# Kernel optimization log

Hardware: AMD Instinct MI355X
Metric: run time of the kernel (lower is better)

The kernel has to match this reference:

```python
import jax, jax.numpy as jnp
import numpy as np

A = 32        # num_agents (nodes per graph block)
B = 128       # batch graphs
N = B * A     # nodes per timestep = 4096
T = 5         # temporal_window_size
K = 16        # num_belief_states
AD = 8        # action_dim
H = 4         # num_attn_heads
DH = 64       # hidden_dim (per GAT head)
D = H * DH    # feature_dim = 256
HD = D // H   # temporal MHA head dim = 64
L = 64        # latent_dim
FIN = K + AD  # discrete node feature dim = 24


def _block_edges():
    # fully connected within each batch block, incl. self loops (PyG GATConv default)
    s = np.repeat(np.arange(A), A)
    d = np.tile(np.arange(A), A)
    off = (np.arange(B) * A)[:, None]
    src = (off + s[None, :]).reshape(-1)
    dst = (off + d[None, :]).reshape(-1)
    return jnp.asarray(np.stack([src, dst]), dtype=jnp.int32)  # [2, B*A*A]


def setup_inputs():
    key = jax.random.key(0)
    ks = jax.random.split(key, 16)
    g = lambda i, shape, s=0.05: jax.random.normal(ks[i], shape, dtype=jnp.float32) * s
    z = lambda shape: jnp.zeros(shape, jnp.float32)
    return {
        'node_feats': g(0, (T, N, FIN), 1.0),
        'edge_index': _block_edges(),
        'gat1_w': g(1, (FIN, D)), 'gat1_asrc': g(2, (H, DH)), 'gat1_adst': g(3, (H, DH)), 'gat1_b': z((D,)),
        'gat2_w': g(4, (D, D)), 'gat2_asrc': g(5, (H, DH)), 'gat2_adst': g(6, (H, DH)), 'gat2_b': z((D,)),
        'wq': g(7, (D, D)), 'bq': z((D,)),
        'wk': g(8, (D, D)), 'bk': z((D,)),
        'wv': g(9, (D, D)), 'bv': z((D,)),
        'wo': g(10, (D, D)), 'bo': z((D,)),
        'lm_w': g(11, (D, L)), 'lm_b': z((L,)),
        'lv_w': g(12, (D, L)), 'lv_b': z((L,)),
        'ap_w': g(13, (L, AD * A)), 'ap_b': z((AD * A,)),
        'bh_w': g(14, (D, K)), 'bh_b': z((K,)),
    }


def _gat_layer(x, W, a_src, a_dst, b, src, dst):
    # PyG GATConv: per-edge additive attention, softmax over incoming edges of dst
    h = (x @ W).reshape(N, H, DH)
    al_s = (h * a_src[None]).sum(-1)                      # [N,H]
    al_d = (h * a_dst[None]).sum(-1)                      # [N,H]
    e = jax.nn.leaky_relu(al_s[src] + al_d[dst], 0.2)     # [E,H]
    m = jax.ops.segment_max(e, dst, num_segments=N)
    p = jnp.exp(e - m[dst])
    zden = jax.ops.segment_sum(p, dst, num_segments=N)
    alpha = p / (zden[dst] + 1e-16)                       # [E,H]
    out = jax.ops.segment_sum(h[src] * alpha[:, :, None], dst, num_segments=N)
    return out.reshape(N, D) + b


def reference(node_feats, edge_index, gat1_w, gat1_asrc, gat1_adst, gat1_b,
              gat2_w, gat2_asrc, gat2_adst, gat2_b,
              wq, bq, wk, bk, wv, bv, wo, bo,
              lm_w, lm_b, lv_w, lv_b, ap_w, ap_b, bh_w, bh_b):
    src, dst = edge_index[0], edge_index[1]

    def gnn(x):  # two GATConv layers + ReLU (dropout inactive at inference)
        x = jax.nn.relu(_gat_layer(x, gat1_w, gat1_asrc, gat1_adst, gat1_b, src, dst))
        x = jax.nn.relu(_gat_layer(x, gat2_w, gat2_asrc, gat2_adst, gat2_b, src, dst))
        return x

    feats = jax.vmap(gnn)(node_feats)          # [T,N,D]
    ego = feats[:, ::A, :]                     # ego node of each block -> [T,B,D]
    seq = jnp.transpose(ego, (1, 0, 2))        # [B,T,D]

    # temporal MultiheadAttention with causal mask (batch_first)
    q = (seq @ wq + bq).reshape(B, T, H, HD)
    k = (seq @ wk + bk).reshape(B, T, H, HD)
    v = (seq @ wv + bv).reshape(B, T, H, HD)
    scores = jnp.einsum('bthd,bshd->bhts', q, k) / jnp.sqrt(jnp.float32(HD))
    causal = jnp.tril(jnp.ones((T, T), bool))
    scores = jnp.where(causal[None, None], scores, jnp.float32(-1e9))
    attn = jax.nn.softmax(scores, axis=-1)
    ctx = jnp.einsum('bhts,bshd->bthd', attn, v).reshape(B, T, D)
    feat = (ctx @ wo + bo)[:, -1]              # last timestep features [B,D]

    mu = feat @ lm_w + lm_b                    # latent_mean
    logvar = feat @ lv_w + lv_b                # latent_logvar
    act = mu @ ap_w + ap_b                     # action_predictor(latent)
    belief = feat @ bh_w + bh_b                # belief_head(features)
    return jnp.concatenate([mu, logvar, act, belief], axis=-1)  # [B, 2L+AD*A+K]
```

## Files before the change

kernel.cpp:

```cpp
#include <hip/hip_runtime.h>

typedef unsigned short u16;
typedef unsigned int u32;
typedef short bf16x8 __attribute__((ext_vector_type(8)));
typedef float f32x4  __attribute__((ext_vector_type(4)));


__device__ __forceinline__ u16 f2b(float f) {
    unsigned u = __float_as_uint(f);
    return (u16)((u + 0x7FFFu + ((u >> 16) & 1u)) >> 16);
}
__device__ __forceinline__ float b2f(u16 u) {
    return __uint_as_float(((unsigned)u) << 16);
}
__device__ __forceinline__ u32 pk2(float a, float b) {
    return (u32)f2b(a) | ((u32)f2b(b) << 16);
}

__global__ __launch_bounds__(256) void prep_kernel(
    const float* __restrict__ w2, u16* __restrict__ w2t,
    const float* __restrict__ w1, u16* __restrict__ w1t)
{
    if (blockIdx.x == 64) {
        const int n = threadIdx.x;
        u32 pk[16];
#pragma unroll
        for (int s = 0; s < 16; ++s) {
            const int k = 2 * s;
            const float lo = (k < 24)     ? w1[k * 256 + n]       : 0.f;
            const float hi = (k + 1 < 24) ? w1[(k + 1) * 256 + n] : 0.f;
            pk[s] = pk2(lo, hi);
        }
        u32* dst = (u32*)(w1t + n * 32);
#pragma unroll
        for (int s = 0; s < 4; ++s)
            *(uint4*)&dst[s * 4] = make_uint4(pk[4*s], pk[4*s+1], pk[4*s+2], pk[4*s+3]);
        return;
    }
    __shared__ float tile[32][33];
    const int bi = blockIdx.x >> 3, bj = blockIdx.x & 7;
    const int r0 = bi * 32, c0 = bj * 32;
    const int lr = threadIdx.x >> 5, lc = threadIdx.x & 31;
    for (int i = lr; i < 32; i += 8)
        tile[i][lc] = w2[(r0 + i) * 256 + c0 + lc];
    __syncthreads();
    for (int i = lr; i < 32; i += 8)
        w2t[(c0 + i) * 256 + r0 + lc] = f2b(tile[lc][i]);
}

__global__ __launch_bounds__(256, 3) void gat12_kernel(
    const float* __restrict__ x, const u16* __restrict__ w1t,
    const float* __restrict__ a1s, const float* __restrict__ a1d,
    const float* __restrict__ b1,
    const u16* __restrict__ w2t, const float* __restrict__ a2s,
    const float* __restrict__ a2d, const float* __restrict__ b2,
    u16* __restrict__ ego,
    const float* __restrict__ wq, const float* __restrict__ wk,
    const float* __restrict__ wv, const float* __restrict__ wo,
    const float* __restrict__ lm_w, const float* __restrict__ lv_w,
    const float* __restrict__ bh_w, const float* __restrict__ ap_w,
    u16* __restrict__ wqkvt, u16* __restrict__ wot,
    u16* __restrict__ headT, u16* __restrict__ apT)
{
    constexpr int HP = 40;
    constexpr int XP = 264;

    __shared__ u16 h1T[256 * HP];
    __shared__ u16 x2s[32 * XP];
    __shared__ u16 alphaT[4 * 32 * HP];
    __shared__ float als2[256], ald2[256];
    __shared__ u16 a1sb[256], a1db[256], a2sb[256], a2db[256];
    __shared__ float alpha0[4][32];

    const int tid = threadIdx.x;

    if (blockIdx.x >= 640) {
        const int bid = blockIdx.x - 640;
        const float* src; u16* dst;
        int C = 256, S = 256, roff = 0, bi, bj;
        if (bid < 192) {
            const int m = bid >> 6, tl = bid & 63;
            src = (m == 0) ? wq : (m == 1) ? wk : wv;
            dst = wqkvt + m * 65536;
            bi = tl >> 3; bj = tl & 7;
        } else if (bid < 256) {
            const int tl = bid - 192;
            src = wo; dst = wot; bi = tl >> 3; bj = tl & 7;
        } else if (bid < 272) {
            const int tl = bid - 256;
            src = lm_w; dst = headT; C = 64; bi = tl >> 1; bj = tl & 1;
        } else if (bid < 288) {
            const int tl = bid - 272;
            src = lv_w; dst = headT; C = 64; roff = 64; bi = tl >> 1; bj = tl & 1;
        } else if (bid < 296) {
            src = bh_w; dst = headT; C = 16; roff = 128; bi = bid - 288; bj = 0;
        } else {
            const int tl = bid - 296;
            src = ap_w; dst = apT; S = 64; bi = tl >> 3; bj = tl & 7;
        }
        float (*tile)[33] = (float(*)[33])h1T;
        const int r0 = bi * 32, c0 = bj * 32;
        const int lr = tid >> 5, lc = tid & 31;
        const int cw = (C - c0 < 32) ? (C - c0) : 32;
        for (int i = lr; i < 32; i += 8)
            if (lc < cw) tile[i][lc] = src[(r0 + i) * C + c0 + lc];
        __syncthreads();
        for (int i = lr; i < cw; i += 8)
            dst[(roff + c0 + i) * S + r0 + lc] = f2b(tile[lc][i]);
        return;
    }

    const int wave = tid >> 6;
    const int l    = tid & 63;
    const int l15  = l & 15;
    const int quad = l >> 4;
    const int t    = blockIdx.x >> 7;
    const int b    = blockIdx.x & 127;
    const long row0 = (long)(t * 4096 + b * 32);

    u16* xs = alphaT;
    if (tid < 128) {
        const int node = tid >> 2, seg = tid & 3;
        u32 pk[4] = {0, 0, 0, 0};
        if (seg < 3) {
            const float* xp = x + row0 * 24 + node * 24 + seg * 8;
            const float4 v0 = *(const float4*)xp;
            const float4 v1 = *(const float4*)(xp + 4);
            pk[0] = pk2(v0.x, v0.y); pk[1] = pk2(v0.z, v0.w);
            pk[2] = pk2(v1.x, v1.y); pk[3] = pk2(v1.z, v1.w);
        }
        *(uint4*)&xs[node * 32 + seg * 8] = make_uint4(pk[0], pk[1], pk[2], pk[3]);
    }
    a1sb[tid] = f2b(a1s[tid]);  a1db[tid] = f2b(a1d[tid]);
    a2sb[tid] = f2b(a2s[tid]);  a2db[tid] = f2b(a2d[tid]);
    __syncthreads();

    {
        const int n0 = wave * 64;
        const bf16x8 a0 = *(const bf16x8*)&xs[(l15)      * 32 + quad * 8];
        const bf16x8 a1 = *(const bf16x8*)&xs[(16 + l15) * 32 + quad * 8];
        f32x4 acc[2][4];
#pragma unroll
        for (int nt = 0; nt < 4; ++nt) {
            const bf16x8 bb = *(const bf16x8*)(w1t + (n0 + nt * 16 + l15) * 32 + quad * 8);
            acc[0][nt] = __builtin_amdgcn_mfma_f32_16x16x32_bf16(a0, bb, (f32x4){0.f,0.f,0.f,0.f}, 0, 0, 0);
            acc[1][nt] = __builtin_amdgcn_mfma_f32_16x16x32_bf16(a1, bb, (f32x4){0.f,0.f,0.f,0.f}, 0, 0, 0);
        }
        __syncthreads();
#pragma unroll
        for (int mt = 0; mt < 2; ++mt)
#pragma unroll
            for (int nt = 0; nt < 4; ++nt) {
                const int col = n0 + nt * 16 + l15;
                *(uint2*)&h1T[col * HP + mt * 16 + quad * 4] =
                    make_uint2(pk2(acc[mt][nt][0], acc[mt][nt][1]),
                               pk2(acc[mt][nt][2], acc[mt][nt][3]));
            }
    }
    __syncthreads();

    {
        const int pair = tid >> 7;
        const int id = tid & 127;
        const int i = id >> 2, hh = id & 3;
        float as = 0.f, ad = 0.f;
        for (int cc = 0; cc < 32; ++cc) {
            const int c = (((cc + tid) & 31) | (pair << 5)) + hh * 64;
            const float hv = b2f(h1T[c * HP + i]);
            as += hv * b2f(a1sb[c]);
            ad += hv * b2f(a1db[c]);
        }
        als2[tid] = as;
        ald2[tid] = ad;
    }
    __syncthreads();

    if (tid < 128) {
        const int hh = tid & 3, dd = tid >> 2;
        const float advv = ald2[tid] + ald2[128 + tid];
        float e[32]; float m = -1e30f;
#pragma unroll
        for (int s = 0; s < 32; ++s) {
            float v = (als2[s * 4 + hh] + als2[128 + s * 4 + hh]) + advv;
            v = v > 0.f ? v : 0.2f * v;
            e[s] = v; m = fmaxf(m, v);
        }
        float sum = 0.f;
#pragma unroll
        for (int s = 0; s < 32; ++s) { float p = __expf(e[s] - m); e[s] = p; sum += p; }
        const float inv = 1.f / (sum + 1e-16f);
        u32 pk[16];
#pragma unroll
        for (int s = 0; s < 16; ++s) pk[s] = pk2(e[2*s] * inv, e[2*s+1] * inv);
        u32* dst = (u32*)&alphaT[(hh * 32 + dd) * HP];
#pragma unroll
        for (int s = 0; s < 4; ++s)
            *(uint4*)&dst[s * 4] = make_uint4(pk[4*s], pk[4*s+1], pk[4*s+2], pk[4*s+3]);
    }
    __syncthreads();

    {
        const int hh = wave;
        bf16x8 af[2];
#pragma unroll
        for (int mt = 0; mt < 2; ++mt)
            af[mt] = *(const bf16x8*)&alphaT[(hh * 32 + mt * 16 + l15) * HP + quad * 8];
        f32x4 acc[2][4];
#pragma unroll
        for (int mt = 0; mt < 2; ++mt)
#pragma unroll
            for (int nt = 0; nt < 4; ++nt) acc[mt][nt] = (f32x4){0.f, 0.f, 0.f, 0.f};
#pragma unroll
        for (int nt = 0; nt < 4; ++nt) {
            const bf16x8 bf = *(const bf16x8*)&h1T[(hh * 64 + nt * 16 + l15) * HP + quad * 8];
            acc[0][nt] = __builtin_amdgcn_mfma_f32_16x16x32_bf16(af[0], bf, acc[0][nt], 0, 0, 0);
            acc[1][nt] = __builtin_amdgcn_mfma_f32_16x16x32_bf16(af[1], bf, acc[1][nt], 0, 0, 0);
        }
#pragma unroll
        for (int mt = 0; mt < 2; ++mt)
#pragma unroll
            for (int nt = 0; nt < 4; ++nt) {
                const int col = hh * 64 + nt * 16 + l15;
                const float bb = b1[col];
#pragma unroll
                for (int r = 0; r < 4; ++r) {
                    const int d = mt * 16 + quad * 4 + r;
                    x2s[d * XP + col] = f2b(fmaxf(acc[mt][nt][r] + bb, 0.f));
                }
            }
    }
    __syncthreads();

    u16* h2s = h1T;
    {
        const int n0 = wave * 64;
        f32x4 acc[2][4];
#pragma unroll
        for (int mt = 0; mt < 2; ++mt)
#pragma unroll
            for (int nt = 0; nt < 4; ++nt) acc[mt][nt] = (f32x4){0.f, 0.f, 0.f, 0.f};
        for (int k0 = 0; k0 < 256; k0 += 32) {
            const int kb = k0 + quad * 8;
            const bf16x8 a0 = *(const bf16x8*)&x2s[(l15)      * XP + kb];
            const bf16x8 a1 = *(const bf16x8*)&x2s[(16 + l15) * XP + kb];
#pragma unroll
            for (int nt = 0; nt < 4; ++nt) {
                const bf16x8 bb = *(const bf16x8*)(w2t + (n0 + nt * 16 + l15) * 256 + kb);
                acc[0][nt] = __builtin_amdgcn_mfma_f32_16x16x32_bf16(a0, bb, acc[0][nt], 0, 0, 0);
                acc[1][nt] = __builtin_amdgcn_mfma_f32_16x16x32_bf16(a1, bb, acc[1][nt], 0, 0, 0);
            }
        }
#pragma unroll
        for (int mt = 0; mt < 2; ++mt)
#pragma unroll
            for (int nt = 0; nt < 4; ++nt) {
                const int col = n0 + nt * 16 + l15;
                *(uint2*)&h2s[col * HP + mt * 16 + quad * 4] =
                    make_uint2(pk2(acc[mt][nt][0], acc[mt][nt][1]),
                               pk2(acc[mt][nt][2], acc[mt][nt][3]));
            }
    }
    __syncthreads();

    {
        const int pair = tid >> 7;
        const int id = tid & 127;
        const int i = id >> 2, hh = id & 3;
        float as = 0.f, ad = 0.f;
        for (int cc = 0; cc < 32; ++cc) {
            const int c = (((cc + tid) & 31) | (pair << 5)) + hh * 64;
            const float hv = b2f(h2s[c * HP + i]);
            as += hv * b2f(a2sb[c]);
            if (i == 0) ad += hv * b2f(a2db[c]);
        }
        als2[tid] = as;
        if (i == 0) ald2[tid] = ad;
    }
    __syncthreads();

    if (tid < 4) {
        const int hh = tid;
        const float advv = ald2[hh] + ald2[128 + hh];
        float e[32]; float m = -1e30f;
#pragma unroll
        for (int s = 0; s < 32; ++s) {
            float v = (als2[s * 4 + hh] + als2[128 + s * 4 + hh]) + advv;
            v = v > 0.f ? v : 0.2f * v;
            e[s] = v; m = fmaxf(m, v);
        }
        float sum = 0.f;
#pragma unroll
        for (int s = 0; s < 32; ++s) { float p = __expf(e[s] - m); e[s] = p; sum += p; }
        const float inv = 1.f / (sum + 1e-16f);
#pragma unroll
        for (int s = 0; s < 32; ++s) alpha0[hh][s] = e[s] * inv;
    }
    __syncthreads();

    {
        const int hh = tid >> 6;
        float av[32];
#pragma unroll
        for (int j = 0; j < 8; ++j)
            *(float4*)&av[j * 4] = *(const float4*)&alpha0[hh][j * 4];
        const u32* hp = (const u32*)&h2s[tid * HP];
        float a = 0.f;
#pragma unroll
        for (int s2 = 0; s2 < 16; ++s2) {
            const u32 u = hp[s2];
            a += av[2 * s2]     * __uint_as_float(u << 16);
            a += av[2 * s2 + 1] * __uint_as_float(u & 0xffff0000u);
        }
        ego[((long)(t * 128 + b)) * 256 + tid] = f2b(fmaxf(a + b2[tid], 0.f));
    }
}

__global__ __launch_bounds__(256) void qkv_kernel(
    const u16* __restrict__ ego, const u16* __restrict__ wqkvt,
    const float* __restrict__ bq, const float* __restrict__ bk,
    const float* __restrict__ bv_, float* __restrict__ qkv)
{
    const int tid  = threadIdx.x;
    const int wave = tid >> 6;
    const int l    = tid & 63;
    const int l15  = l & 15;
    const int quad = l >> 4;
    int gx, gy;
    if (blockIdx.x < 20)      { gy = 1; gx = blockIdx.x; }
    else if (blockIdx.x < 40) { gy = 2; gx = blockIdx.x - 20; }
    else                      { gy = 0; gx = 16 + (blockIdx.x - 40); }
    const int r0 = gx * 32;
    const int n0 = wave * 64;
    const u16* wsrc = wqkvt + gy * 65536;
    const float* bias = (gy == 0) ? bq : (gy == 1) ? bk : bv_;

    f32x4 acc[2][4];
#pragma unroll
    for (int mt = 0; mt < 2; ++mt)
#pragma unroll
        for (int nt = 0; nt < 4; ++nt) acc[mt][nt] = (f32x4){0.f, 0.f, 0.f, 0.f};

    for (int k0 = 0; k0 < 256; k0 += 32) {
        const int kb = k0 + quad * 8;
        const bf16x8 a0 = *(const bf16x8*)(ego + (r0 + l15)      * 256 + kb);
        const bf16x8 a1 = *(const bf16x8*)(ego + (r0 + 16 + l15) * 256 + kb);
#pragma unroll
        for (int nt = 0; nt < 4; ++nt) {
            const bf16x8 bb = *(const bf16x8*)(wsrc + (n0 + nt * 16 + l15) * 256 + kb);
            acc[0][nt] = __builtin_amdgcn_mfma_f32_16x16x32_bf16(a0, bb, acc[0][nt], 0, 0, 0);
            acc[1][nt] = __builtin_amdgcn_mfma_f32_16x16x32_bf16(a1, bb, acc[1][nt], 0, 0, 0);
        }
    }
#pragma unroll
    for (int mt = 0; mt < 2; ++mt)
#pragma unroll
        for (int nt = 0; nt < 4; ++nt)
#pragma unroll
            for (int r = 0; r < 4; ++r) {
                const int row = r0 + mt * 16 + quad * 4 + r;
                const int col = n0 + nt * 16 + l15;
                qkv[(long)row * 768 + gy * 256 + col] = acc[mt][nt][r] + bias[col];
            }
}

__global__ __launch_bounds__(256) void attn_tail_kernel(
    const float* __restrict__ qkv,
    const u16* __restrict__ wot, const u16* __restrict__ headT,
    const u16* __restrict__ apT,
    const float* __restrict__ bo,
    const float* __restrict__ lm_b, const float* __restrict__ lv_b,
    const float* __restrict__ bh_b, const float* __restrict__ ap_b,
    float* __restrict__ out)
{
    constexpr int FP = 264;
    constexpr int MP = 72;
    __shared__ float scl[16][20];
    __shared__ u16 fs[16 * FP];
    __shared__ u16 ffs[16 * FP];
    __shared__ u16 mus[16 * MP];

    const int tid  = threadIdx.x;
    const int wave = tid >> 6;
    const int l    = tid & 63;
    const int l15  = l & 15;
    const int quad = l >> 4;
    const int b0   = blockIdx.x * 16;

    for (int id = tid; id < 320; id += 256) {
        const int bl = id / 20, r = id % 20, h = r / 5, s = r % 5;
        const float* qp = qkv + (long)(512 + b0 + bl) * 768 + h * 64;
        const float* kp = qkv + (long)(s * 128 + b0 + bl) * 768 + 256 + h * 64;
        float acc = 0.f;
        for (int c = 0; c < 64; c += 4) {
            const float4 qv = *(const float4*)(qp + c);
            const float4 kv = *(const float4*)(kp + c);
            acc += qv.x * kv.x + qv.y * kv.y + qv.z * kv.z + qv.w * kv.w;
        }
        scl[bl][r] = acc * 0.125f;
    }
    __syncthreads();

    if (tid < 64) {
        const int bl = tid >> 2, h = tid & 3;
        float m = -1e30f;
        for (int s = 0; s < 5; ++s) m = fmaxf(m, scl[bl][h * 5 + s]);
        float p[5], sum = 0.f;
        for (int s = 0; s < 5; ++s) { p[s] = __expf(scl[bl][h * 5 + s] - m); sum += p[s]; }
        for (int s = 0; s < 5; ++s) scl[bl][h * 5 + s] = p[s] / sum;
    }
    __syncthreads();

    {
        const int col = tid, h = col >> 6;
        for (int bl = 0; bl < 16; ++bl) {
            float c = 0.f;
#pragma unroll
            for (int s = 0; s < 5; ++s)
                c += scl[bl][h * 5 + s] * qkv[(long)(s * 128 + b0 + bl) * 768 + 512 + col];
            fs[bl * FP + col] = f2b(c);
        }
    }
    __syncthreads();

    {
        const int n0 = wave * 64;
        f32x4 acc[4];
#pragma unroll
        for (int nt = 0; nt < 4; ++nt) acc[nt] = (f32x4){0.f, 0.f, 0.f, 0.f};
        for (int k0 = 0; k0 < 256; k0 += 32) {
            const int kb = k0 + quad * 8;
            const bf16x8 a = *(const bf16x8*)&fs[l15 * FP + kb];
#pragma unroll
            for (int nt = 0; nt < 4; ++nt) {
                const bf16x8 bb = *(const bf16x8*)(wot + (n0 + nt * 16 + l15) * 256 + kb);
                acc[nt] = __builtin_amdgcn_mfma_f32_16x16x32_bf16(a, bb, acc[nt], 0, 0, 0);
            }
        }
#pragma unroll
        for (int nt = 0; nt < 4; ++nt) {
            const int col = n0 + nt * 16 + l15;
            const float bb = bo[col];
#pragma unroll
            for (int r = 0; r < 4; ++r)
                ffs[(quad * 4 + r) * FP + col] = f2b(acc[nt][r] + bb);
        }
    }
    __syncthreads();

    for (int nt = wave; nt < 9; nt += 4) {
        const int n0 = nt * 16;
        f32x4 acc = (f32x4){0.f, 0.f, 0.f, 0.f};
        for (int k0 = 0; k0 < 256; k0 += 32) {
            const int kb = k0 + quad * 8;
            const bf16x8 a  = *(const bf16x8*)&ffs[l15 * FP + kb];
            const bf16x8 bb = *(const bf16x8*)(headT + (n0 + l15) * 256 + kb);
            acc = __builtin_amdgcn_mfma_f32_16x16x32_bf16(a, bb, acc, 0, 0, 0);
        }
        const int col = n0 + l15;
#pragma unroll
        for (int r = 0; r < 4; ++r) {
            const int row = quad * 4 + r;
            float v = acc[r];
            if (col < 64) {
                v += lm_b[col];
                out[(long)(b0 + row) * 400 + col] = v;
                mus[row * MP + col] = f2b(v);
            } else if (col < 128) {
                v += lv_b[col - 64];
                out[(long)(b0 + row) * 400 + col] = v;
            } else {
                v += bh_b[col - 128];
                out[(long)(b0 + row) * 400 + 256 + col] = v;
            }
        }
    }
    __syncthreads();

#pragma unroll
    for (int i = 0; i < 4; ++i) {
        const int n0 = (wave * 4 + i) * 16;
        f32x4 acc = (f32x4){0.f, 0.f, 0.f, 0.f};
#pragma unroll
        for (int k0 = 0; k0 < 64; k0 += 32) {
            const int kb = k0 + quad * 8;
            const bf16x8 a  = *(const bf16x8*)&mus[l15 * MP + kb];
            const bf16x8 bb = *(const bf16x8*)(apT + (n0 + l15) * 64 + kb);
            acc = __builtin_amdgcn_mfma_f32_16x16x32_bf16(a, bb, acc, 0, 0, 0);
        }
        const int col = n0 + l15;
        const float bb = ap_b[col];
#pragma unroll
        for (int r = 0; r < 4; ++r) {
            const int row = quad * 4 + r;
            out[(long)(b0 + row) * 400 + 128 + col] = acc[r] + bb;
        }
    }
}

extern "C" void kernel_launch(void* const* d_in, const int* in_sizes, int n_in,
                              void* d_out, int out_size, void* d_ws, size_t ws_size,
                              hipStream_t stream)
{
    const float* node_feats = (const float*)d_in[0];
    const float* g1w  = (const float*)d_in[2];
    const float* g1as = (const float*)d_in[3];
    const float* g1ad = (const float*)d_in[4];
    const float* g1b  = (const float*)d_in[5];
    const float* g2w  = (const float*)d_in[6];
    const float* g2as = (const float*)d_in[7];
    const float* g2ad = (const float*)d_in[8];
    const float* g2b  = (const float*)d_in[9];
    const float* wq = (const float*)d_in[10]; const float* bq = (const float*)d_in[11];
    const float* wk = (const float*)d_in[12]; const float* bk = (const float*)d_in[13];
    const float* wv = (const float*)d_in[14]; const float* bv = (const float*)d_in[15];
    const float* wo = (const float*)d_in[16]; const float* bo = (const float*)d_in[17];
    const float* lm_w = (const float*)d_in[18]; const float* lm_b = (const float*)d_in[19];
    const float* lv_w = (const float*)d_in[20]; const float* lv_b = (const float*)d_in[21];
    const float* ap_w = (const float*)d_in[22]; const float* ap_b = (const float*)d_in[23];
    const float* bh_w = (const float*)d_in[24]; const float* bh_b = (const float*)d_in[25];

    char* ws = (char*)d_ws;
    u16*   ego   = (u16*)ws;
    u16*   w2t   = (u16*)(ws + 327680);
    u16*   w1t   = (u16*)(ws + 458752);
    u16*   wqkvt = (u16*)(ws + 475136);
    float* qkv   = (float*)(ws + 868352);
    u16*   wot   = (u16*)(ws + 2834432);
    u16*   headT = (u16*)(ws + 2965504);
    u16*   apT   = (u16*)(ws + 3039232);

    prep_kernel<<<65, 256, 0, stream>>>(g2w, w2t, g1w, w1t);
    gat12_kernel<<<952, 256, 0, stream>>>(node_feats, w1t, g1as, g1ad, g1b,
                                          w2t, g2as, g2ad, g2b, ego,
                                          wq, wk, wv, wo, lm_w, lv_w, bh_w, ap_w,
                                          wqkvt, wot, headT, apT);
    qkv_kernel<<<44, 256, 0, stream>>>(ego, wqkvt, bq, bk, bv, qkv);
    attn_tail_kernel<<<8, 256, 0, stream>>>(qkv, wot, headT, apT, bo,
                                            lm_b, lv_b, bh_b, ap_b, (float*)d_out);
}
```

Measured before the change: 156.9 us.

## Fuse QKV projection and attention tail into one per-graph kernel, shrink GAT LDS

Measured after the change: 162.2 us. 1.03x slower.

```diff
diff --git a/kernel.cpp b/kernel.cpp
--- a/kernel.cpp
+++ b/kernel.cpp
@@ -48,7 +48,7 @@
         w2t[(c0 + i) * 256 + r0 + lc] = f2b(tile[lc][i]);
 }
 
-__global__ __launch_bounds__(256, 3) void gat12_kernel(
+__global__ __launch_bounds__(256, 4) void gat12_kernel(
     const float* __restrict__ x, const u16* __restrict__ w1t,
     const float* __restrict__ a1s, const float* __restrict__ a1d,
     const float* __restrict__ b1,
@@ -65,13 +65,10 @@
     constexpr int HP = 40;
     constexpr int XP = 264;
 
-    __shared__ u16 h1T[256 * HP];
-    __shared__ u16 x2s[32 * XP];
-    __shared__ u16 alphaT[4 * 32 * HP];
-    __shared__ float als2[256], ald2[256];
-    __shared__ u16 a1sb[256], a1db[256], a2sb[256], a2db[256];
-    __shared__ float alpha0[4][32];
-
+    __shared__ __align__(16) u16 h1T[256 * HP];
+    __shared__ __align__(16) u16 x2s[32 * XP];
+    __shared__ float als[128], ald[128];
+    __shared__ __align__(16) u16 avec[1024];
     const int tid = threadIdx.x;
 
     if (blockIdx.x >= 640) {
@@ -110,6 +107,10 @@
         return;
     }
 
+    u16* xs     = x2s;
+    u16* alphaT = x2s;
+    float* alpha0 = (float*)avec;
+
     const int wave = tid >> 6;
     const int l    = tid & 63;
     const int l15  = l & 15;
@@ -118,7 +119,6 @@
     const int b    = blockIdx.x & 127;
     const long row0 = (long)(t * 4096 + b * 32);
 
-    u16* xs = alphaT;
     if (tid < 128) {
         const int node = tid >> 2, seg = tid & 3;
         u32 pk[4] = {0, 0, 0, 0};
@@ -131,8 +131,10 @@
         }
         *(uint4*)&xs[node * 32 + seg * 8] = make_uint4(pk[0], pk[1], pk[2], pk[3]);
     }
-    a1sb[tid] = f2b(a1s[tid]);  a1db[tid] = f2b(a1d[tid]);
-    a2sb[tid] = f2b(a2s[tid]);  a2db[tid] = f2b(a2d[tid]);
+    avec[tid]       = f2b(a1s[tid]);
+    avec[256 + tid] = f2b(a1d[tid]);
+    avec[512 + tid] = f2b(a2s[tid]);
+    avec[768 + tid] = f2b(a2d[tid]);
     __syncthreads();
 
     {
@@ -146,7 +148,6 @@
             acc[0][nt] = __builtin_amdgcn_mfma_f32_16x16x32_bf16(a0, bb, (f32x4){0.f,0.f,0.f,0.f}, 0, 0, 0);
             acc[1][nt] = __builtin_amdgcn_mfma_f32_16x16x32_bf16(a1, bb, (f32x4){0.f,0.f,0.f,0.f}, 0, 0, 0);
         }
-        __syncthreads();
 #pragma unroll
         for (int mt = 0; mt < 2; ++mt)
 #pragma unroll
@@ -159,29 +160,27 @@
     }
     __syncthreads();
 
-    {
-        const int pair = tid >> 7;
-        const int id = tid & 127;
-        const int i = id >> 2, hh = id & 3;
+    if (tid < 128) {
+        const int i = tid >> 2, hh = tid & 3;
         float as = 0.f, ad = 0.f;
-        for (int cc = 0; cc < 32; ++cc) {
-            const int c = (((cc + tid) & 31) | (pair << 5)) + hh * 64;
+        for (int cc = 0; cc < 64; ++cc) {
+            const int c = hh * 64 + ((cc + tid) & 63);
             const float hv = b2f(h1T[c * HP + i]);
-            as += hv * b2f(a1sb[c]);
-            ad += hv * b2f(a1db[c]);
-        }
-        als2[tid] = as;
-        ald2[tid] = ad;
+            as += hv * b2f(avec[c]);
+            ad += hv * b2f(avec[256 + c]);
+        }
+        als[tid] = as;
+        ald[tid] = ad;
     }
     __syncthreads();
 
     if (tid < 128) {
         const int hh = tid & 3, dd = tid >> 2;
-        const float advv = ald2[tid] + ald2[128 + tid];
+        const float advv = ald[tid];
         float e[32]; float m = -1e30f;
 #pragma unroll
         for (int s = 0; s < 32; ++s) {
-            float v = (als2[s * 4 + hh] + als2[128 + s * 4 + hh]) + advv;
+            float v = als[s * 4 + hh] + advv;
             v = v > 0.f ? v : 0.2f * v;
             e[s] = v; m = fmaxf(m, v);
         }
@@ -205,6 +204,7 @@
 #pragma unroll
         for (int mt = 0; mt < 2; ++mt)
             af[mt] = *(const bf16x8*)&alphaT[(hh * 32 + mt * 16 + l15) * HP + quad * 8];
+        __syncthreads();
         f32x4 acc[2][4];
 #pragma unroll
         for (int mt = 0; mt < 2; ++mt)
@@ -262,29 +262,27 @@
     }
     __syncthreads();
 
-    {
-        const int pair = tid >> 7;
-        const int id = tid & 127;
-        const int i = id >> 2, hh = id & 3;
+    if (tid < 128) {
+        const int i = tid >> 2, hh = tid & 3;
         float as = 0.f, ad = 0.f;
-        for (int cc = 0; cc < 32; ++cc) {
-            const int c = (((cc + tid) & 31) | (pair << 5)) + hh * 64;
+        for (int cc = 0; cc < 64; ++cc) {
+            const int c = hh * 64 + ((cc + tid) & 63);
             const float hv = b2f(h2s[c * HP + i]);
-            as += hv * b2f(a2sb[c]);
-            if (i == 0) ad += hv * b2f(a2db[c]);
-        }
-        als2[tid] = as;
-        if (i == 0) ald2[tid] = ad;
+            as += hv * b2f(avec[512 + c]);
+            if (i == 0) ad += hv * b2f(avec[768 + c]);
+        }
+        als[tid] = as;
+        if (i == 0) ald[tid] = ad;
     }
     __syncthreads();
 
     if (tid < 4) {
         const int hh = tid;
-        const float advv = ald2[hh] + ald2[128 + hh];
+        const float advv = ald[hh];
         float e[32]; float m = -1e30f;
 #pragma unroll
         for (int s = 0; s < 32; ++s) {
-            float v = (als2[s * 4 + hh] + als2[128 + s * 4 + hh]) + advv;
+            float v = als[s * 4 + hh] + advv;
             v = v > 0.f ? v : 0.2f * v;
             e[s] = v; m = fmaxf(m, v);
         }
@@ -293,7 +291,7 @@
         for (int s = 0; s < 32; ++s) { float p = __expf(e[s] - m); e[s] = p; sum += p; }
         const float inv = 1.f / (sum + 1e-16f);
 #pragma unroll
-        for (int s = 0; s < 32; ++s) alpha0[hh][s] = e[s] * inv;
+        for (int s = 0; s < 32; ++s) alpha0[hh * 32 + s] = e[s] * inv;
     }
     __syncthreads();
 
@@ -302,7 +300,7 @@
         float av[32];
 #pragma unroll
         for (int j = 0; j < 8; ++j)
-            *(float4*)&av[j * 4] = *(const float4*)&alpha0[hh][j * 4];
+            *(float4*)&av[j * 4] = *(const float4*)&alpha0[hh * 32 + j * 4];
         const u32* hp = (const u32*)&h2s[tid * HP];
         float a = 0.f;
 #pragma unroll
@@ -315,56 +313,10 @@
     }
 }
 
-__global__ __launch_bounds__(256) void qkv_kernel(
+__global__ __launch_bounds__(256) void post_kernel(
     const u16* __restrict__ ego, const u16* __restrict__ wqkvt,
     const float* __restrict__ bq, const float* __restrict__ bk,
-    const float* __restrict__ bv_, float* __restrict__ qkv)
-{
-    const int tid  = threadIdx.x;
-    const int wave = tid >> 6;
-    const int l    = tid & 63;
-    const int l15  = l & 15;
-    const int quad = l >> 4;
-    int gx, gy;
-    if (blockIdx.x < 20)      { gy = 1; gx = blockIdx.x; }
-    else if (blockIdx.x < 40) { gy = 2; gx = blockIdx.x - 20; }
-    else                      { gy = 0; gx = 16 + (blockIdx.x - 40); }
-    const int r0 = gx * 32;
-    const int n0 = wave * 64;
-    const u16* wsrc = wqkvt + gy * 65536;
-    const float* bias = (gy == 0) ? bq : (gy == 1) ? bk : bv_;
-
-    f32x4 acc[2][4];
-#pragma unroll
-    for (int mt = 0; mt < 2; ++mt)
-#pragma unroll
-        for (int nt = 0; nt < 4; ++nt) acc[mt][nt] = (f32x4){0.f, 0.f, 0.f, 0.f};
-
-    for (int k0 = 0; k0 < 256; k0 += 32) {
-        const int kb = k0 + quad * 8;
-        const bf16x8 a0 = *(const bf16x8*)(ego + (r0 + l15)      * 256 + kb);
-        const bf16x8 a1 = *(const bf16x8*)(ego + (r0 + 16 + l15) * 256 + kb);
-#pragma unroll
-        for (int nt = 0; nt < 4; ++nt) {
-            const bf16x8 bb = *(const bf16x8*)(wsrc + (n0 + nt * 16 + l15) * 256 + kb);
-            acc[0][nt] = __builtin_amdgcn_mfma_f32_16x16x32_bf16(a0, bb, acc[0][nt], 0, 0, 0);
-            acc[1][nt] = __builtin_amdgcn_mfma_f32_16x16x32_bf16(a1, bb, acc[1][nt], 0, 0, 0);
-        }
-    }
-#pragma unroll
-    for (int mt = 0; mt < 2; ++mt)
-#pragma unroll
-        for (int nt = 0; nt < 4; ++nt)
-#pragma unroll
-            for (int r = 0; r < 4; ++r) {
-                const int row = r0 + mt * 16 + quad * 4 + r;
-                const int col = n0 + nt * 16 + l15;
-                qkv[(long)row * 768 + gy * 256 + col] = acc[mt][nt][r] + bias[col];
-            }
-}
-
-__global__ __launch_bounds__(256) void attn_tail_kernel(
-    const float* __restrict__ qkv,
+    const float* __restrict__ bv_,
     const u16* __restrict__ wot, const u16* __restrict__ headT,
     const u16* __restrict__ apT,
     const float* __restrict__ bo,
@@ -372,54 +324,99 @@
     const float* __restrict__ bh_b, const float* __restrict__ ap_b,
     float* __restrict__ out)
 {
-    constexpr int FP = 264;
+    constexpr int EP = 264;
     constexpr int MP = 72;
-    __shared__ float scl[16][20];
-    __shared__ u16 fs[16 * FP];
-    __shared__ u16 ffs[16 * FP];
-    __shared__ u16 mus[16 * MP];
+    __shared__ __align__(16) u16 egoS[16 * EP];
+    __shared__ float q4[256];
+    __shared__ __align__(16) float kk[5 * 256];
+    __shared__ float vv[5 * 256];
+    __shared__ float scl[20];
+
+    u16* mus = (u16*)kk;
 
     const int tid  = threadIdx.x;
     const int wave = tid >> 6;
     const int l    = tid & 63;
     const int l15  = l & 15;
     const int quad = l >> 4;
-    const int b0   = blockIdx.x * 16;
-
-    for (int id = tid; id < 320; id += 256) {
-        const int bl = id / 20, r = id % 20, h = r / 5, s = r % 5;
-        const float* qp = qkv + (long)(512 + b0 + bl) * 768 + h * 64;
-        const float* kp = qkv + (long)(s * 128 + b0 + bl) * 768 + 256 + h * 64;
-        float acc = 0.f;
+    const int b    = blockIdx.x;
+
+    for (int idx = tid; idx < 16 * 33; idx += 256) {
+        const int row = idx / 33, seg = idx % 33;
+        uint4 v = make_uint4(0, 0, 0, 0);
+        if (row < 5 && seg < 32)
+            v = *(const uint4*)(ego + ((long)(row * 128 + b)) * 256 + seg * 8);
+        *(uint4*)&egoS[row * EP + seg * 8] = v;
+    }
+    __syncthreads();
+
+    {
+        f32x4 acc[12];
+#pragma unroll
+        for (int nt = 0; nt < 12; ++nt) acc[nt] = (f32x4){0.f, 0.f, 0.f, 0.f};
+        for (int k0 = 0; k0 < 256; k0 += 32) {
+            const int kb = k0 + quad * 8;
+            const bf16x8 a = *(const bf16x8*)&egoS[l15 * EP + kb];
+#pragma unroll
+            for (int nt = 0; nt < 12; ++nt) {
+                const int col = wave * 192 + nt * 16 + l15;
+                const bf16x8 bb = *(const bf16x8*)(wqkvt + (long)col * 256 + kb);
+                acc[nt] = __builtin_amdgcn_mfma_f32_16x16x32_bf16(a, bb, acc[nt], 0, 0, 0);
+            }
+        }
+#pragma unroll
+        for (int nt = 0; nt < 12; ++nt) {
+            const int col = wave * 192 + nt * 16 + l15;
+            const float bias = (col < 256) ? bq[col]
+                              : (col < 512) ? bk[col - 256] : bv_[col - 512];
+#pragma unroll
+            for (int r = 0; r < 4; ++r) {
+                const int m = quad * 4 + r;
+                if (m < 5) {
+                    const float v = acc[nt][r] + bias;
+                    if (col < 256)      { if (m == 4) q4[col] = v; }
+                    else if (col < 512) kk[m * 256 + col - 256] = v;
+                    else                vv[m * 256 + col - 512] = v;
+                }
+            }
+        }
+    }
+    __syncthreads();
+
+    if (tid < 20) {
+        const int hh = tid / 5, ss = tid % 5;
+        float sc = 0.f;
         for (int c = 0; c < 64; c += 4) {
-            const float4 qv = *(const float4*)(qp + c);
-            const float4 kv = *(const float4*)(kp + c);
-            acc += qv.x * kv.x + qv.y * kv.y + qv.z * kv.z + qv.w * kv.w;
-        }
-        scl[bl][r] = acc * 0.125f;
-    }
-    __syncthreads();
-
-    if (tid < 64) {
-        const int bl = tid >> 2, h = tid & 3;
+            const float4 qv = *(const float4*)&q4[hh * 64 + c];
+            const float4 kv = *(const float4*)&kk[ss * 256 + hh * 64 + c];
+            sc += qv.x * kv.x + qv.y * kv.y + qv.z * kv.z + qv.w * kv.w;
+        }
+        scl[tid] = sc * 0.125f;
+    }
+    __syncthreads();
+
+    if (tid < 4) {
         float m = -1e30f;
-        for (int s = 0; s < 5; ++s) m = fmaxf(m, scl[bl][h * 5 + s]);
+        for (int s = 0; s < 5; ++s) m = fmaxf(m, scl[tid * 5 + s]);
         float p[5], sum = 0.f;
-        for (int s = 0; s < 5; ++s) { p[s] = __expf(scl[bl][h * 5 + s] - m); sum += p[s]; }
-        for (int s = 0; s < 5; ++s) scl[bl][h * 5 + s] = p[s] / sum;
-    }
-    __syncthreads();
-
-    {
-        const int col = tid, h = col >> 6;
-        for (int bl = 0; bl < 16; ++bl) {
-            float c = 0.f;
-#pragma unroll
-            for (int s = 0; s < 5; ++s)
-                c += scl[bl][h * 5 + s] * qkv[(long)(s * 128 + b0 + bl) * 768 + 512 + col];
-            fs[bl * FP + col] = f2b(c);
-        }
-    }
+        for (int s = 0; s < 5; ++s) { p[s] = __expf(scl[tid * 5 + s] - m); sum += p[s]; }
+        for (int s = 0; s < 5; ++s) scl[tid * 5 + s] = p[s] / sum;
+    }
+    __syncthreads();
+
+    {
+        const int hh = tid >> 6;
+        float c = 0.f;
+#pragma unroll
+        for (int s = 0; s < 5; ++s) c += scl[hh * 5 + s] * vv[s * 256 + tid];
+        egoS[tid] = f2b(c);
+    }
+    for (int idx = tid; idx < 4 * 33; idx += 256) {
+        const int row = 1 + idx / 33, seg = idx % 33;
+        *(uint4*)&egoS[row * EP + seg * 8] = make_uint4(0, 0, 0, 0);
+    }
+    for (int idx = tid; idx < 144; idx += 256)
+        *(uint4*)&mus[idx * 8] = make_uint4(0, 0, 0, 0);
     __syncthreads();
 
     {
@@ -429,48 +426,45 @@
         for (int nt = 0; nt < 4; ++nt) acc[nt] = (f32x4){0.f, 0.f, 0.f, 0.f};
         for (int k0 = 0; k0 < 256; k0 += 32) {
             const int kb = k0 + quad * 8;
-            const bf16x8 a = *(const bf16x8*)&fs[l15 * FP + kb];
+            const bf16x8 a = *(const bf16x8*)&egoS[l15 * EP + kb];
 #pragma unroll
             for (int nt = 0; nt < 4; ++nt) {
                 const bf16x8 bb = *(const bf16x8*)(wot + (n0 + nt * 16 + l15) * 256 + kb);
                 acc[nt] = __builtin_amdgcn_mfma_f32_16x16x32_bf16(a, bb, acc[nt], 0, 0, 0);
             }
         }
-#pragma unroll
-        for (int nt = 0; nt < 4; ++nt) {
-            const int col = n0 + nt * 16 + l15;
-            const float bb = bo[col];
-#pragma unroll
-            for (int r = 0; r < 4; ++r)
-                ffs[(quad * 4 + r) * FP + col] = f2b(acc[nt][r] + bb);
-        }
-    }
-    __syncthreads();
-
+        __syncthreads();
+        if (quad == 0) {
+#pragma unroll
+            for (int nt = 0; nt < 4; ++nt) {
+                const int col = n0 + nt * 16 + l15;
+                egoS[col] = f2b(acc[nt][0] + bo[col]);
+            }
+        }
+    }
+    __syncthreads();
+
+    float* ob = out + (long)b * 400;
     for (int nt = wave; nt < 9; nt += 4) {
         const int n0 = nt * 16;
         f32x4 acc = (f32x4){0.f, 0.f, 0.f, 0.f};
         for (int k0 = 0; k0 < 256; k0 += 32) {
             const int kb = k0 + quad * 8;
-            const bf16x8 a  = *(const bf16x8*)&ffs[l15 * FP + kb];
+            const bf16x8 a  = *(const bf16x8*)&egoS[l15 * EP + kb];
             const bf16x8 bb = *(const bf16x8*)(headT + (n0 + l15) * 256 + kb);
             acc = __builtin_amdgcn_mfma_f32_16x16x32_bf16(a, bb, acc, 0, 0, 0);
         }
-        const int col = n0 + l15;
-#pragma unroll
-        for (int r = 0; r < 4; ++r) {
-            const int row = quad * 4 + r;
-            float v = acc[r];
+        if (quad == 0) {
+            const int col = n0 + l15;
+            float v = acc[0];
             if (col < 64) {
                 v += lm_b[col];
-                out[(long)(b0 + row) * 400 + col] = v;
-                mus[row * MP + col] = f2b(v);
+                ob[col] = v;
+                mus[col] = f2b(v);
             } else if (col < 128) {
-                v += lv_b[col - 64];
-                out[(long)(b0 + row) * 400 + col] = v;
+                ob[col] = v + lv_b[col - 64];
             } else {
-                v += bh_b[col - 128];
-                out[(long)(b0 + row) * 400 + 256 + col] = v;
+                ob[256 + col] = v + bh_b[col - 128];
             }
         }
     }
@@ -487,12 +481,9 @@
             const bf16x8 bb = *(const bf16x8*)(apT + (n0 + l15) * 64 + kb);
             acc = __builtin_amdgcn_mfma_f32_16x16x32_bf16(a, bb, acc, 0, 0, 0);
         }
-        const int col = n0 + l15;
-        const float bb = ap_b[col];
-#pragma unroll
-        for (int r = 0; r < 4; ++r) {
-            const int row = quad * 4 + r;
-            out[(long)(b0 + row) * 400 + 128 + col] = acc[r] + bb;
+        if (quad == 0) {
+            const int col = n0 + l15;
+            ob[128 + col] = acc[0] + ap_b[col];
         }
     }
 }
@@ -524,17 +515,16 @@
     u16*   w2t   = (u16*)(ws + 327680);
     u16*   w1t   = (u16*)(ws + 458752);
     u16*   wqkvt = (u16*)(ws + 475136);
-    float* qkv   = (float*)(ws + 868352);
-    u16*   wot   = (u16*)(ws + 2834432);
-    u16*   headT = (u16*)(ws + 2965504);
-    u16*   apT   = (u16*)(ws + 3039232);
+    u16*   wot   = (u16*)(ws + 868352);
+    u16*   headT = (u16*)(ws + 999424);
+    u16*   apT   = (u16*)(ws + 1073152);
 
     prep_kernel<<<65, 256, 0, stream>>>(g2w, w2t, g1w, w1t);
     gat12_kernel<<<952, 256, 0, stream>>>(node_feats, w1t, g1as, g1ad, g1b,
                                           w2t, g2as, g2ad, g2b, ego,
                                           wq, wk, wv, wo, lm_w, lv_w, bh_w, ap_w,
                                           wqkvt, wot, headT, apT);
-    qkv_kernel<<<44, 256, 0, stream>>>(ego, wqkvt, bq, bk, bv, qkv);
-    attn_tail_kernel<<<8, 256, 0, stream>>>(qkv, wot, headT, apT, bo,
-                                            lm_b, lv_b, bh_b, ap_b, (float*)d_out);
-}
+    post_kernel<<<128, 256, 0, stream>>>(ego, wqkvt, bq, bk, bv,
+                                         wot, headT, apT, bo,
+                                         lm_b, lv_b, bh_b, ap_b, (float*)d_out);
+}
```

## Shrink GAT kernel shared memory via buffer aliasing to allow four blocks per CU

Applied to the files above, without the earlier changes.

Result: no change. 159.8 us (median of 2 runs) (+1.9%).

```diff
diff --git a/kernel.cpp b/kernel.cpp
--- a/kernel.cpp
+++ b/kernel.cpp
@@ -48,7 +48,7 @@
         w2t[(c0 + i) * 256 + r0 + lc] = f2b(tile[lc][i]);
 }
 
-__global__ __launch_bounds__(256, 3) void gat12_kernel(
+__global__ __launch_bounds__(256, 4) void gat12_kernel(
     const float* __restrict__ x, const u16* __restrict__ w1t,
     const float* __restrict__ a1s, const float* __restrict__ a1d,
     const float* __restrict__ b1,
@@ -65,13 +65,10 @@
     constexpr int HP = 40;
     constexpr int XP = 264;
 
-    __shared__ u16 h1T[256 * HP];
-    __shared__ u16 x2s[32 * XP];
-    __shared__ u16 alphaT[4 * 32 * HP];
-    __shared__ float als2[256], ald2[256];
-    __shared__ u16 a1sb[256], a1db[256], a2sb[256], a2db[256];
-    __shared__ float alpha0[4][32];
-
+    __shared__ __align__(16) u16 h1T[256 * HP];
+    __shared__ __align__(16) u16 x2s[32 * XP];
+    __shared__ float als[128], ald[128];
+    __shared__ __align__(16) u16 avec[1024];
     const int tid = threadIdx.x;
 
     if (blockIdx.x >= 640) {
@@ -110,6 +107,10 @@
         return;
     }
 
+    u16* xs     = x2s;
+    u16* alphaT = x2s;
+    float* alpha0 = (float*)avec;
+
     const int wave = tid >> 6;
     const int l    = tid & 63;
     const int l15  = l & 15;
@@ -118,7 +119,6 @@
     const int b    = blockIdx.x & 127;
     const long row0 = (long)(t * 4096 + b * 32);
 
-    u16* xs = alphaT;
     if (tid < 128) {
         const int node = tid >> 2, seg = tid & 3;
         u32 pk[4] = {0, 0, 0, 0};
@@ -131,8 +131,10 @@
         }
         *(uint4*)&xs[node * 32 + seg * 8] = make_uint4(pk[0], pk[1], pk[2], pk[3]);
     }
-    a1sb[tid] = f2b(a1s[tid]);  a1db[tid] = f2b(a1d[tid]);
-    a2sb[tid] = f2b(a2s[tid]);  a2db[tid] = f2b(a2d[tid]);
+    avec[tid]       = f2b(a1s[tid]);
+    avec[256 + tid] = f2b(a1d[tid]);
+    avec[512 + tid] = f2b(a2s[tid]);
+    avec[768 + tid] = f2b(a2d[tid]);
     __syncthreads();
 
     {
@@ -146,7 +148,6 @@
             acc[0][nt] = __builtin_amdgcn_mfma_f32_16x16x32_bf16(a0, bb, (f32x4){0.f,0.f,0.f,0.f}, 0, 0, 0);
             acc[1][nt] = __builtin_amdgcn_mfma_f32_16x16x32_bf16(a1, bb, (f32x4){0.f,0.f,0.f,0.f}, 0, 0, 0);
         }
-        __syncthreads();
 #pragma unroll
         for (int mt = 0; mt < 2; ++mt)
 #pragma unroll
@@ -160,28 +161,25 @@
     __syncthreads();
 
     {
-        const int pair = tid >> 7;
         const int id = tid & 127;
         const int i = id >> 2, hh = id & 3;
-        float as = 0.f, ad = 0.f;
-        for (int cc = 0; cc < 32; ++cc) {
-            const int c = (((cc + tid) & 31) | (pair << 5)) + hh * 64;
-            const float hv = b2f(h1T[c * HP + i]);
-            as += hv * b2f(a1sb[c]);
-            ad += hv * b2f(a1db[c]);
-        }
-        als2[tid] = as;
-        ald2[tid] = ad;
+        const u16* av = avec + ((tid < 128) ? 0 : 256);
+        float acc = 0.f;
+        for (int cc = 0; cc < 64; ++cc) {
+            const int c = hh * 64 + ((cc + tid) & 63);
+            acc += b2f(h1T[c * HP + i]) * b2f(av[c]);
+        }
+        if (tid < 128) als[id] = acc; else ald[id] = acc;
     }
     __syncthreads();
 
     if (tid < 128) {
         const int hh = tid & 3, dd = tid >> 2;
-        const float advv = ald2[tid] + ald2[128 + tid];
+        const float advv = ald[tid];
         float e[32]; float m = -1e30f;
 #pragma unroll
         for (int s = 0; s < 32; ++s) {
-            float v = (als2[s * 4 + hh] + als2[128 + s * 4 + hh]) + advv;
+            float v = als[s * 4 + hh] + advv;
             v = v > 0.f ? v : 0.2f * v;
             e[s] = v; m = fmaxf(m, v);
         }
@@ -205,6 +203,7 @@
 #pragma unroll
         for (int mt = 0; mt < 2; ++mt)
             af[mt] = *(const bf16x8*)&alphaT[(hh * 32 + mt * 16 + l15) * HP + quad * 8];
+        __syncthreads();
         f32x4 acc[2][4];
 #pragma unroll
         for (int mt = 0; mt < 2; ++mt)
@@ -263,28 +262,27 @@
     __syncthreads();
 
     {
-        const int pair = tid >> 7;
         const int id = tid & 127;
         const int i = id >> 2, hh = id & 3;
-        float as = 0.f, ad = 0.f;
-        for (int cc = 0; cc < 32; ++cc) {
-            const int c = (((cc + tid) & 31) | (pair << 5)) + hh * 64;
-            const float hv = b2f(h2s[c * HP + i]);
-            as += hv * b2f(a2sb[c]);
-            if (i == 0) ad += hv * b2f(a2db[c]);
-        }
-        als2[tid] = as;
-        if (i == 0) ald2[tid] = ad;
+        if (tid < 128 || id < 4) {
+            const u16* av = avec + ((tid < 128) ? 512 : 768);
+            float acc = 0.f;
+            for (int cc = 0; cc < 64; ++cc) {
+                const int c = hh * 64 + ((cc + tid) & 63);
+                acc += b2f(h2s[c * HP + i]) * b2f(av[c]);
+            }
+            if (tid < 128) als[id] = acc; else ald[id] = acc;
+        }
     }
     __syncthreads();
 
     if (tid < 4) {
         const int hh = tid;
-        const float advv = ald2[hh] + ald2[128 + hh];
+        const float advv = ald[hh];
         float e[32]; float m = -1e30f;
 #pragma unroll
         for (int s = 0; s < 32; ++s) {
-            float v = (als2[s * 4 + hh] + als2[128 + s * 4 + hh]) + advv;
+            float v = als[s * 4 + hh] + advv;
             v = v > 0.f ? v : 0.2f * v;
             e[s] = v; m = fmaxf(m, v);
         }
@@ -293,7 +291,7 @@
         for (int s = 0; s < 32; ++s) { float p = __expf(e[s] - m); e[s] = p; sum += p; }
         const float inv = 1.f / (sum + 1e-16f);
 #pragma unroll
-        for (int s = 0; s < 32; ++s) alpha0[hh][s] = e[s] * inv;
+        for (int s = 0; s < 32; ++s) alpha0[hh * 32 + s] = e[s] * inv;
     }
     __syncthreads();
 
@@ -302,7 +300,7 @@
         float av[32];
 #pragma unroll
         for (int j = 0; j < 8; ++j)
-            *(float4*)&av[j * 4] = *(const float4*)&alpha0[hh][j * 4];
+            *(float4*)&av[j * 4] = *(const float4*)&alpha0[hh * 32 + j * 4];
         const u32* hp = (const u32*)&h2s[tid * HP];
         float a = 0.f;
 #pragma unroll
```
